# Optimization experiments

Hardware: AMD Instinct MI355X
Metric: run time of the kernel (lower is better)

Reference implementation:

```python
import jax, jax.numpy as jnp
import numpy as np

B, N, DM, H, FF = 8, 2048, 1024, 16, 4096
D = DM // H // 2  # head_dim = 32
LAMBDA_INIT = 0.8 - 0.6 * float(np.exp(-0.3 * 1.0))  # layer_num=1


def _layernorm(x, g, b, eps=1e-5):
    mu = jnp.mean(x, axis=-1, keepdims=True)
    var = jnp.mean(jnp.square(x - mu), axis=-1, keepdims=True)
    return (x - mu) * jax.lax.rsqrt(var + eps) * g + b


def _rmsnorm(x, eps=1e-5):
    return x * jax.lax.rsqrt(jnp.mean(x * x, axis=-1, keepdims=True) + eps)


def _diff_attn(x, Wq, Wk, Wv, lq1, lq2, lk1, lk2, Wo, bo):
    b, n, d = x.shape
    scale = D ** -0.5
    # rearrange 'b n (h d q) -> b n (q h) d'
    q = (x @ Wq.T).reshape(b, n, H, D, 2).transpose(0, 1, 4, 2, 3).reshape(b, n, 2 * H, D) * scale
    k = (x @ Wk.T).reshape(b, n, H, D, 2).transpose(0, 1, 4, 2, 3).reshape(b, n, 2 * H, D)
    # rearrange 'b n (h d) -> b h n d' with d = 2*head_dim
    v = (x @ Wv.T).reshape(b, n, H, 2 * D).transpose(0, 2, 1, 3)
    # per-position head-vs-head scores: [b, n, 2H, 2H]
    att = jnp.einsum('bnqd,bnkd->bnqk', q, k)
    att = jnp.nan_to_num(att)
    att = jax.nn.softmax(att.astype(jnp.float32), axis=-1)
    lam = jnp.exp(jnp.sum(lq1 * lk1)) - jnp.exp(jnp.sum(lq2 * lk2)) + LAMBDA_INIT
    # rearrange 'b n (q h) (k a) -> q k b n h a'; take [0,0] - lam*[1,1]
    att6 = att.reshape(b, n, 2, H, 2, H)
    att2 = att6[:, :, 0, :, 0, :] - lam * att6[:, :, 1, :, 1, :]  # [b,n,h,a]
    out = jnp.einsum('bnah,bhnd->bnad', att2, v)  # [b,n,H,2D]
    out = _rmsnorm(out) * (1.0 - LAMBDA_INIT)
    out = out.reshape(b, n, d)
    return out @ Wo.T + bo


def setup_inputs() -> dict:
    key = jax.random.key(0)
    ks = jax.random.split(key, 12)
    p = lambda k, sh, s=0.02: jax.random.normal(k, sh, jnp.float32) * s
    return {
        'x': jax.random.normal(ks[0], (B, N, DM), jnp.float32),
        'Wq': p(ks[1], (DM, DM)), 'Wk': p(ks[2], (DM, DM)), 'Wv': p(ks[3], (DM, DM)),
        'lq1': p(ks[4], (D,), 0.1), 'lq2': p(ks[5], (D,), 0.1),
        'lk1': p(ks[6], (D,), 0.1), 'lk2': p(ks[7], (D,), 0.1),
        'Wo': p(ks[8], (DM, DM)), 'bo': jnp.zeros((DM,), jnp.float32),
        'ln1_g': jnp.ones((DM,), jnp.float32), 'ln1_b': jnp.zeros((DM,), jnp.float32),
        'ln2_g': jnp.ones((DM,), jnp.float32), 'ln2_b': jnp.zeros((DM,), jnp.float32),
        'W1': p(ks[9], (FF, DM)), 'b1': jnp.zeros((FF,), jnp.float32),
        'W2': p(ks[10], (DM, FF)), 'b2': jnp.zeros((DM,), jnp.float32),
    }


def reference(x, Wq, Wk, Wv, lq1, lq2, lk1, lk2, Wo, bo, ln1_g, ln1_b, ln2_g, ln2_b, W1, b1, W2, b2):
    # norm_first=True, use_gate=False, dropout=0 (eval), wo_ffn=False
    skip = x
    h = _layernorm(x, ln1_g, ln1_b)
    src2 = _diff_attn(h, Wq, Wk, Wv, lq1, lq2, lk1, lk2, Wo, bo)
    conn = skip + src2
    skip2 = conn
    h2 = _layernorm(conn, ln2_g, ln2_b)
    src3 = jax.nn.relu(h2 @ W1.T + b1) @ W2.T + b2
    return skip2 + src3
```

## Files before the change

kernel.cpp:

```cpp
#include <hip/hip_runtime.h>
#include <cstdint>

#define DM    1024
#define NHEAD 16
#define FFDIM 4096
#define MROWS 16384
#define QKVS  3072

static constexpr float LAMBDA_INIT_F = 0.3555090675909693f;
static constexpr float ONE_MINUS_LI  = 1.0f - 0.3555090675909693f;
static constexpr float QSCALE        = 0.17677669529663687f;

typedef __attribute__((ext_vector_type(8))) short bf16x8;
typedef __attribute__((ext_vector_type(4))) float f32x4;

__device__ __forceinline__ unsigned short f2bf(float f) {
    union { float f; unsigned int i; } w; w.f = f;
    unsigned int x = w.i;
    return (unsigned short)((x + 0x7fffu + ((x >> 16) & 1u)) >> 16);
}
__device__ __forceinline__ float bf2f(unsigned short u) {
    union { unsigned int i; float f; } w; w.i = ((unsigned int)u) << 16; return w.f;
}

__device__ __forceinline__ void load_lds16(const void* gptr, void* lptr) {
    __builtin_amdgcn_global_load_lds(
        (const __attribute__((address_space(1))) unsigned int*)gptr,
        (__attribute__((address_space(3))) unsigned int*)lptr, 16, 0, 0);
}

__global__ __launch_bounds__(256) void cvt6_kernel(const float* __restrict__ Wq,
                                                   const float* __restrict__ Wk,
                                                   const float* __restrict__ Wv,
                                                   const float* __restrict__ Wo,
                                                   const float* __restrict__ W1,
                                                   const float* __restrict__ W2,
                                                   unsigned short* __restrict__ wqkv,
                                                   unsigned short* __restrict__ wo,
                                                   unsigned short* __restrict__ w1,
                                                   unsigned short* __restrict__ w2)
{
    const int b = blockIdx.x;
    const float* src;
    unsigned short* dst;
    int off;
    if (b < 3072)      { src = (b < 1024) ? Wq : (b < 2048) ? Wk : Wv;
                         dst = wqkv + (b >> 10) * (DM * DM);
                         off = (b & 1023) * 1024; }
    else if (b < 4096) { src = Wo; dst = wo; off = (b - 3072) * 1024; }
    else if (b < 8192) { src = W1; dst = w1; off = (b - 4096) * 1024; }
    else               { src = W2; dst = w2; off = (b - 8192) * 1024; }
    const int i = off + threadIdx.x * 4;
    const float4 v = *(const float4*)&src[i];
    ushort4 o;
    o.x = f2bf(v.x); o.y = f2bf(v.y); o.z = f2bf(v.z); o.w = f2bf(v.w);
    *(ushort4*)&dst[i] = o;
}

__global__ __launch_bounds__(256) void ln_kernel(const float* __restrict__ xin,
                                                 const float* __restrict__ g,
                                                 const float* __restrict__ b,
                                                 unsigned short* __restrict__ out)
{
    const int row = blockIdx.x;
    const int tid = threadIdx.x;
    const float* xr = xin + (size_t)row * DM;
    float v[4];
    #pragma unroll
    for (int i = 0; i < 4; ++i) v[i] = xr[tid + 256 * i];
    float s1 = v[0] + v[1] + v[2] + v[3];
    float s2 = v[0]*v[0] + v[1]*v[1] + v[2]*v[2] + v[3]*v[3];
    #pragma unroll
    for (int off = 32; off > 0; off >>= 1) {
        s1 += __shfl_down(s1, off);
        s2 += __shfl_down(s2, off);
    }
    __shared__ float red[8];
    const int wv = tid >> 6;
    if ((tid & 63) == 0) { red[wv] = s1; red[4 + wv] = s2; }
    __syncthreads();
    s1 = red[0] + red[1] + red[2] + red[3];
    s2 = red[4] + red[5] + red[6] + red[7];
    const float mean = s1 * (1.0f / DM);
    const float var  = s2 * (1.0f / DM) - mean * mean;
    const float inv  = rsqrtf(var + 1e-5f);
    #pragma unroll
    for (int i = 0; i < 4; ++i) {
        const int c = tid + 256 * i;
        out[(size_t)row * DM + c] = f2bf((v[i] - mean) * inv * g[c] + b[c]);
    }
}

template<int EPI>
__global__ __launch_bounds__(512, 2) void gemm256(const unsigned short* __restrict__ A,
                                                  const unsigned short* __restrict__ W,
                                                  void* __restrict__ Cout,
                                                  const float* __restrict__ bias,
                                                  const float* __restrict__ resid,
                                                  int M, int N, int K, int ldb)
{
    __shared__ __align__(16) unsigned short Al[2][256][64];
    __shared__ __align__(16) unsigned short Bl[2][256][64];

    const int tid  = threadIdx.x;
    const int lane = tid & 63;
    const int wv   = tid >> 6;
    const int l15  = lane & 15;
    const int q4   = lane >> 4;
    const int wg   = wv >> 2;
    const int cg   = wv & 3;
    const int m0   = blockIdx.y * 256;
    const int n0   = blockIdx.x * 256;
    const int KT   = K >> 6;

    const int sr = tid >> 3;
    const int sc = (tid & 7) ^ (sr & 7);
    const unsigned short* gA = A + (size_t)(m0 + sr) * K   + sc * 8;
    const unsigned short* gB = W + (size_t)(n0 + sr) * ldb + sc * 8;
    const size_t aH = (size_t)128 * K;
    const size_t bH = (size_t)128 * ldb;
    const size_t aC = (size_t)64 * K;
    const size_t bC = (size_t)64 * ldb;
    unsigned short* lA = &Al[0][0][0] + wv * 512;
    unsigned short* lB = &Bl[0][0][0] + wv * 512;

#define STG_A(boff, hoff, gp) do { \
    load_lds16((gp),      lA + (boff) + (hoff)); \
    load_lds16((gp) + aC, lA + (boff) + (hoff) + 4096); } while (0)
#define STG_B(boff, hoff, gp) do { \
    load_lds16((gp),      lB + (boff) + (hoff)); \
    load_lds16((gp) + bC, lB + (boff) + (hoff) + 4096); } while (0)

    STG_A(0, 0,    gA);
    STG_B(0, 0,    gB);
    STG_A(0, 8192, gA + aH);
    STG_B(0, 8192, gB + bH);
    if (KT > 1) {
        STG_A(16384, 0,    gA + 64);
        STG_B(16384, 0,    gB + 64);
        STG_A(16384, 8192, gA + aH + 64);
        asm volatile("s_waitcnt vmcnt(6)" ::: "memory");
    } else {
        asm volatile("s_waitcnt vmcnt(0)" ::: "memory");
    }
    __builtin_amdgcn_s_barrier();
    __builtin_amdgcn_sched_barrier(0);

    const int so0 = ( q4      ^ (l15 & 7)) * 8;
    const int so1 = ((q4 + 4) ^ (l15 & 7)) * 8;
    const unsigned short* rA = &Al[0][wg * 64 + l15][0];
    const unsigned short* rB = &Bl[0][cg * 32 + l15][0];

    const f32x4 fz = {0.f, 0.f, 0.f, 0.f};
    f32x4 acc[8][4];
    #pragma unroll
    for (int i = 0; i < 8; ++i)
        #pragma unroll
        for (int j = 0; j < 4; ++j) acc[i][j] = fz;

    bf16x8 a[4][2], b0[2][2], b1[2][2];

    for (int t = 0; t < KT; ++t) {
        const int bo = (t & 1) << 14;
        const int bn = bo ^ 16384;
        const int k1 = (t + 1) << 6;
        const int k2 = (t + 2) << 6;

        #pragma unroll
        for (int mf = 0; mf < 4; ++mf) {
            a[mf][0] = *(const bf16x8*)&rA[bo + mf * 1024 + so0];
            a[mf][1] = *(const bf16x8*)&rA[bo + mf * 1024 + so1];
        }
        #pragma unroll
        for (int nf = 0; nf < 2; ++nf) {
            b0[nf][0] = *(const bf16x8*)&rB[bo + nf * 1024 + so0];
            b0[nf][1] = *(const bf16x8*)&rB[bo + nf * 1024 + so1];
        }
        if (t + 1 < KT) STG_B(bn, 8192, gB + bH + k1);
        __builtin_amdgcn_s_barrier();
        __builtin_amdgcn_sched_barrier(0);
        __builtin_amdgcn_s_setprio(1);
        #pragma unroll
        for (int mf = 0; mf < 4; ++mf)
            #pragma unroll
            for (int nf = 0; nf < 2; ++nf) {
                acc[mf][nf] = __builtin_amdgcn_mfma_f32_16x16x32_bf16(a[mf][0], b0[nf][0], acc[mf][nf], 0, 0, 0);
                acc[mf][nf] = __builtin_amdgcn_mfma_f32_16x16x32_bf16(a[mf][1], b0[nf][1], acc[mf][nf], 0, 0, 0);
            }
        __builtin_amdgcn_s_setprio(0);
        __builtin_amdgcn_s_barrier();
        __builtin_amdgcn_sched_barrier(0);

        #pragma unroll
        for (int nf = 0; nf < 2; ++nf) {
            b1[nf][0] = *(const bf16x8*)&rB[bo + 8192 + nf * 1024 + so0];
            b1[nf][1] = *(const bf16x8*)&rB[bo + 8192 + nf * 1024 + so1];
        }
        if (t + 2 < KT) STG_A(bo, 0, gA + k2);
        __builtin_amdgcn_s_barrier();
        __builtin_amdgcn_sched_barrier(0);
        __builtin_amdgcn_s_setprio(1);
        #pragma unroll
        for (int mf = 0; mf < 4; ++mf)
            #pragma unroll
            for (int nf = 0; nf < 2; ++nf) {
                acc[mf][2 + nf] = __builtin_amdgcn_mfma_f32_16x16x32_bf16(a[mf][0], b1[nf][0], acc[mf][2 + nf], 0, 0, 0);
                acc[mf][2 + nf] = __builtin_amdgcn_mfma_f32_16x16x32_bf16(a[mf][1], b1[nf][1], acc[mf][2 + nf], 0, 0, 0);
            }
        __builtin_amdgcn_s_setprio(0);
        __builtin_amdgcn_s_barrier();
        __builtin_amdgcn_sched_barrier(0);

        #pragma unroll
        for (int mf = 0; mf < 4; ++mf) {
            a[mf][0] = *(const bf16x8*)&rA[bo + 8192 + mf * 1024 + so0];
            a[mf][1] = *(const bf16x8*)&rA[bo + 8192 + mf * 1024 + so1];
        }
        if (t + 2 < KT) STG_B(bo, 0, gB + k2);
        __builtin_amdgcn_s_barrier();
        __builtin_amdgcn_sched_barrier(0);
        __builtin_amdgcn_s_setprio(1);
        #pragma unroll
        for (int mf = 0; mf < 4; ++mf)
            #pragma unroll
            for (int nf = 0; nf < 2; ++nf) {
                acc[4 + mf][nf] = __builtin_amdgcn_mfma_f32_16x16x32_bf16(a[mf][0], b0[nf][0], acc[4 + mf][nf], 0, 0, 0);
                acc[4 + mf][nf] = __builtin_amdgcn_mfma_f32_16x16x32_bf16(a[mf][1], b0[nf][1], acc[4 + mf][nf], 0, 0, 0);
            }
        __builtin_amdgcn_s_setprio(0);
        __builtin_amdgcn_s_barrier();
        __builtin_amdgcn_sched_barrier(0);

        if (t + 2 < KT) STG_A(bo, 8192, gA + aH + k2);
        __builtin_amdgcn_s_barrier();
        __builtin_amdgcn_sched_barrier(0);
        __builtin_amdgcn_s_setprio(1);
        #pragma unroll
        for (int mf = 0; mf < 4; ++mf)
            #pragma unroll
            for (int nf = 0; nf < 2; ++nf) {
                acc[4 + mf][2 + nf] = __builtin_amdgcn_mfma_f32_16x16x32_bf16(a[mf][0], b1[nf][0], acc[4 + mf][2 + nf], 0, 0, 0);
                acc[4 + mf][2 + nf] = __builtin_amdgcn_mfma_f32_16x16x32_bf16(a[mf][1], b1[nf][1], acc[4 + mf][2 + nf], 0, 0, 0);
            }
        __builtin_amdgcn_s_setprio(0);
        if (t + 2 < KT) {
            asm volatile("s_waitcnt vmcnt(6)" ::: "memory");
        } else if (t + 2 == KT) {
            asm volatile("s_waitcnt vmcnt(0)" ::: "memory");
        }
        if (t + 1 < KT) {
            __builtin_amdgcn_s_barrier();
            __builtin_amdgcn_sched_barrier(0);
        }
    }
#undef STG_A
#undef STG_B

    #pragma unroll
    for (int hm = 0; hm < 2; ++hm)
    #pragma unroll
    for (int mf = 0; mf < 4; ++mf)
    #pragma unroll
    for (int hb = 0; hb < 2; ++hb)
    #pragma unroll
    for (int nf = 0; nf < 2; ++nf)
    #pragma unroll
    for (int rr = 0; rr < 4; ++rr) {
        const int m = m0 + hm * 128 + wg * 64 + mf * 16 + q4 * 4 + rr;
        const int n = n0 + hb * 128 + cg * 32 + nf * 16 + l15;
        const size_t off = (size_t)m * N + n;
        float c = acc[hm * 4 + mf][hb * 2 + nf][rr];
        if (EPI == 0) {
            ((unsigned short*)Cout)[off] = f2bf(c);
        } else if (EPI == 1) {
            ((float*)Cout)[off] = c + bias[n] + resid[off];
        } else if (EPI == 2) {
            ((unsigned short*)Cout)[off] = f2bf(fmaxf(c + bias[n], 0.f));
        } else {
            ((float*)Cout)[off] = c + resid[off];
        }
    }
}

__global__ __launch_bounds__(256) void attn_pos(const unsigned short* __restrict__ qkv,
                                                const float* __restrict__ lq1,
                                                const float* __restrict__ lq2,
                                                const float* __restrict__ lk1,
                                                const float* __restrict__ lk2,
                                                unsigned short* __restrict__ outg)
{
    __shared__ __align__(16) float q2[4][32][36];
    __shared__ __align__(16) float k2[4][32][36];
    __shared__ __align__(16) float v2[4][16][64];
    __shared__ float att2[4][16][17];

    const int tid  = threadIdx.x;
    const int wave = tid >> 6;
    const int lane = tid & 63;
    const int pos  = blockIdx.x * 4 + wave;

    float s1 = 0.f, s2 = 0.f;
    #pragma unroll
    for (int i = 0; i < 32; ++i) {
        s1 += lq1[i] * lk1[i];
        s2 += lq2[i] * lk2[i];
    }
    const float lam = __expf(s1) - __expf(s2) + LAMBDA_INIT_F;

    const unsigned short* qrow = qkv + (size_t)pos * QKVS;
    const unsigned short* krow = qrow + DM;
    const unsigned short* vrow = qrow + 2 * DM;

    unsigned short tq[16], tk[16], tv[16];
    *(uint4*)&tq[0] = *(const uint4*)&qrow[lane * 16];
    *(uint4*)&tq[8] = *(const uint4*)&qrow[lane * 16 + 8];
    *(uint4*)&tk[0] = *(const uint4*)&krow[lane * 16];
    *(uint4*)&tk[8] = *(const uint4*)&krow[lane * 16 + 8];
    *(uint4*)&tv[0] = *(const uint4*)&vrow[lane * 16];
    *(uint4*)&tv[8] = *(const uint4*)&vrow[lane * 16 + 8];

    #pragma unroll
    for (int jj = 0; jj < 16; ++jj) {
        const int c  = lane * 16 + jj;
        const int h  = c >> 6;
        const int d  = (c >> 1) & 31;
        const int qi = c & 1;
        q2[wave][qi * 16 + h][d] = bf2f(tq[jj]) * QSCALE;
        k2[wave][qi * 16 + h][d] = bf2f(tk[jj]);
        v2[wave][c >> 6][c & 63] = bf2f(tv[jj]);
    }
    __syncthreads();

    const int qh = lane & 31, half = lane >> 5;
    float qreg[32];
    #pragma unroll
    for (int d4 = 0; d4 < 32; d4 += 4) {
        const f32x4 t = *(const f32x4*)&q2[wave][qh][d4];
        qreg[d4] = t[0]; qreg[d4+1] = t[1]; qreg[d4+2] = t[2]; qreg[d4+3] = t[3];
    }
    float p[16];
    #pragma unroll
    for (int jj = 0; jj < 16; ++jj) {
        const float* kr = &k2[wave][half * 16 + jj][0];
        float a = 0.f;
        #pragma unroll
        for (int d4 = 0; d4 < 32; d4 += 4) {
            const f32x4 kv = *(const f32x4*)&kr[d4];
            a += qreg[d4]*kv[0] + qreg[d4+1]*kv[1] + qreg[d4+2]*kv[2] + qreg[d4+3]*kv[3];
        }
        p[jj] = a;
    }

    float mx = p[0];
    #pragma unroll
    for (int jj = 1; jj < 16; ++jj) mx = fmaxf(mx, p[jj]);
    mx = fmaxf(mx, __shfl_xor(mx, 32));
    float sum = 0.f;
    #pragma unroll
    for (int jj = 0; jj < 16; ++jj) { p[jj] = __expf(p[jj] - mx); sum += p[jj]; }
    sum += __shfl_xor(sum, 32);
    const float inv = 1.0f / sum;

    if (half == 0 && qh < 16) {
        #pragma unroll
        for (int jj = 0; jj < 16; ++jj) att2[wave][qh][jj] = p[jj] * inv;
    }
    __syncthreads();
    if (half == 1 && qh >= 16) {
        const int a = qh - 16;
        #pragma unroll
        for (int jj = 0; jj < 16; ++jj) att2[wave][a][jj] -= lam * p[jj] * inv;
    }
    __syncthreads();

    const int a   = lane & 15;
    const int ddb = (lane >> 4) * 16;
    float areg[16];
    #pragma unroll
    for (int h = 0; h < 16; ++h) areg[h] = att2[wave][a][h];
    float o[16];
    #pragma unroll
    for (int j = 0; j < 16; ++j) o[j] = 0.f;
    #pragma unroll
    for (int h = 0; h < 16; ++h) {
        #pragma unroll
        for (int j4 = 0; j4 < 16; j4 += 4) {
            const f32x4 vv = *(const f32x4*)&v2[wave][h][ddb + j4];
            o[j4]   += areg[h] * vv[0];
            o[j4+1] += areg[h] * vv[1];
            o[j4+2] += areg[h] * vv[2];
            o[j4+3] += areg[h] * vv[3];
        }
    }

    float ss = 0.f;
    #pragma unroll
    for (int j = 0; j < 16; ++j) ss += o[j] * o[j];
    ss += __shfl_xor(ss, 16);
    ss += __shfl_xor(ss, 32);
    const float scl = rsqrtf(ss * (1.0f / 64.0f) + 1e-5f) * ONE_MINUS_LI;

    unsigned short ob[16];
    #pragma unroll
    for (int j = 0; j < 16; ++j) ob[j] = f2bf(o[j] * scl);
    unsigned short* orow = outg + (size_t)pos * DM + a * 64 + ddb;
    *(uint4*)&orow[0] = *(const uint4*)&ob[0];
    *(uint4*)&orow[8] = *(const uint4*)&ob[8];
}

extern "C" void kernel_launch(void* const* d_in, const int* in_sizes, int n_in,
                              void* d_out, int out_size, void* d_ws, size_t ws_size,
                              hipStream_t stream)
{
    const float* x   = (const float*)d_in[0];
    const float* Wq  = (const float*)d_in[1];
    const float* Wk  = (const float*)d_in[2];
    const float* Wv  = (const float*)d_in[3];
    const float* lq1 = (const float*)d_in[4];
    const float* lq2 = (const float*)d_in[5];
    const float* lk1 = (const float*)d_in[6];
    const float* lk2 = (const float*)d_in[7];
    const float* Wo  = (const float*)d_in[8];
    const float* bo  = (const float*)d_in[9];
    const float* g1  = (const float*)d_in[10];
    const float* be1 = (const float*)d_in[11];
    const float* g2  = (const float*)d_in[12];
    const float* be2 = (const float*)d_in[13];
    const float* W1  = (const float*)d_in[14];
    const float* b1  = (const float*)d_in[15];
    const float* W2  = (const float*)d_in[16];
    const float* b2  = (const float*)d_in[17];
    (void)in_sizes; (void)n_in; (void)out_size;

    const size_t MB = 1ull << 20;
    char* ws = (char*)d_ws;
    unsigned short* wqkv = (unsigned short*)(ws);
    unsigned short* wo   = (unsigned short*)(ws + 6 * MB);
    unsigned short* w1   = (unsigned short*)(ws + 8 * MB);
    unsigned short* w2   = (unsigned short*)(ws + 16 * MB);
    unsigned short* h    = (unsigned short*)(ws + 24 * MB);
    unsigned short* qkv  = (unsigned short*)(ws + 56 * MB);
    float*          conn = (float*)(ws + 56 * MB);
    unsigned short* attn = h;
    unsigned short* h2   = (unsigned short*)(ws + 120 * MB);
    unsigned short* t    = (unsigned short*)(ws + 152 * MB);

    int nf = 1;
    while (nf < 16 && 152 * MB + (size_t)MROWS * (FFDIM / nf) * 2 > ws_size) nf <<= 1;
    const int FC = FFDIM / nf;

    const dim3 b256(256), b512(512);

    cvt6_kernel<<<12288, b256, 0, stream>>>(Wq, Wk, Wv, Wo, W1, W2, wqkv, wo, w1, w2);

    ln_kernel<<<MROWS, b256, 0, stream>>>(x, g1, be1, h);

    gemm256<0><<<dim3(QKVS / 256, MROWS / 256), b512, 0, stream>>>(
        h, wqkv, qkv, nullptr, nullptr, MROWS, QKVS, DM, DM);

    attn_pos<<<MROWS / 4, b256, 0, stream>>>(qkv, lq1, lq2, lk1, lk2, attn);

    gemm256<1><<<dim3(DM / 256, MROWS / 256), b512, 0, stream>>>(
        attn, wo, conn, bo, x, MROWS, DM, DM, DM);

    ln_kernel<<<MROWS, b256, 0, stream>>>(conn, g2, be2, h2);

    for (int c = 0; c < nf; ++c) {
        gemm256<2><<<dim3(FC / 256, MROWS / 256), b512, 0, stream>>>(
            h2, w1 + (size_t)c * FC * DM, t, b1 + c * FC, nullptr, MROWS, FC, DM, DM);
        if (c == 0)
            gemm256<1><<<dim3(DM / 256, MROWS / 256), b512, 0, stream>>>(
                t, w2 + (size_t)c * FC, (float*)d_out, b2, conn, MROWS, DM, FC, FFDIM);
        else
            gemm256<4><<<dim3(DM / 256, MROWS / 256), b512, 0, stream>>>(
                t, w2 + (size_t)c * FC, (float*)d_out, nullptr, (const float*)d_out, MROWS, DM, FC, FFDIM);
    }
}
```

Baseline: 707.8 us.

## Swizzle GEMM block order and drop barriers between LDS reads and MFMA phases

Remaps the linear workgroup index into eight interleaved groups so that concurrently running blocks share A/B tiles and get better L2 reuse. It removes the s_barrier and sched_barrier that sat between each LDS fragment load / global-to-LDS stage and the MFMA cluster that follows, halving the barrier count per k-step. It also reorders the LDS fragment loads so the first MFMA's operands arrive first. Without those barriers the compiler can move loads and MFMAs across phases, and correctness now depends on the remaining barriers still ordering LDS writes against reads.

Result: no change. 698.4 us (-1.3%).

```diff
diff --git a/kernel.cpp b/kernel.cpp
--- a/kernel.cpp
+++ b/kernel.cpp
@@ -109,9 +109,21 @@
     const int q4   = lane >> 4;
     const int wg   = wv >> 2;
     const int cg   = wv & 3;
-    const int m0   = blockIdx.y * 256;
-    const int n0   = blockIdx.x * 256;
-    const int KT   = K >> 6;
+
+    int bx = blockIdx.x, by = blockIdx.y;
+    {
+        const int gx  = gridDim.x;
+        const int nwg = gx * gridDim.y;
+        if ((nwg & 7) == 0) {
+            const int lin = by * gx + bx;
+            const int swz = (lin & 7) * (nwg >> 3) + (lin >> 3);
+            bx = swz % gx;
+            by = swz / gx;
+        }
+    }
+    const int m0 = by * 256;
+    const int n0 = bx * 256;
+    const int KT = K >> 6;
 
     const int sr = tid >> 3;
     const int sc = (tid & 7) ^ (sr & 7);
@@ -166,19 +178,19 @@
         const int k1 = (t + 1) << 6;
         const int k2 = (t + 2) << 6;
 
-        #pragma unroll
-        for (int mf = 0; mf < 4; ++mf) {
-            a[mf][0] = *(const bf16x8*)&rA[bo + mf * 1024 + so0];
-            a[mf][1] = *(const bf16x8*)&rA[bo + mf * 1024 + so1];
-        }
-        #pragma unroll
-        for (int nf = 0; nf < 2; ++nf) {
-            b0[nf][0] = *(const bf16x8*)&rB[bo + nf * 1024 + so0];
-            b0[nf][1] = *(const bf16x8*)&rB[bo + nf * 1024 + so1];
-        }
+        a[0][0]  = *(const bf16x8*)&rA[bo + 0 * 1024 + so0];
+        b0[0][0] = *(const bf16x8*)&rB[bo + 0 * 1024 + so0];
+        a[0][1]  = *(const bf16x8*)&rA[bo + 0 * 1024 + so1];
+        b0[0][1] = *(const bf16x8*)&rB[bo + 0 * 1024 + so1];
+        b0[1][0] = *(const bf16x8*)&rB[bo + 1 * 1024 + so0];
+        b0[1][1] = *(const bf16x8*)&rB[bo + 1 * 1024 + so1];
+        a[1][0]  = *(const bf16x8*)&rA[bo + 1 * 1024 + so0];
+        a[1][1]  = *(const bf16x8*)&rA[bo + 1 * 1024 + so1];
+        a[2][0]  = *(const bf16x8*)&rA[bo + 2 * 1024 + so0];
+        a[2][1]  = *(const bf16x8*)&rA[bo + 2 * 1024 + so1];
+        a[3][0]  = *(const bf16x8*)&rA[bo + 3 * 1024 + so0];
+        a[3][1]  = *(const bf16x8*)&rA[bo + 3 * 1024 + so1];
         if (t + 1 < KT) STG_B(bn, 8192, gB + bH + k1);
-        __builtin_amdgcn_s_barrier();
-        __builtin_amdgcn_sched_barrier(0);
         __builtin_amdgcn_s_setprio(1);
         #pragma unroll
         for (int mf = 0; mf < 4; ++mf)
@@ -191,14 +203,11 @@
         __builtin_amdgcn_s_barrier();
         __builtin_amdgcn_sched_barrier(0);
 
-        #pragma unroll
-        for (int nf = 0; nf < 2; ++nf) {
-            b1[nf][0] = *(const bf16x8*)&rB[bo + 8192 + nf * 1024 + so0];
-            b1[nf][1] = *(const bf16x8*)&rB[bo + 8192 + nf * 1024 + so1];
-        }
+        b1[0][0] = *(const bf16x8*)&rB[bo + 8192 + 0 * 1024 + so0];
+        b1[0][1] = *(const bf16x8*)&rB[bo + 8192 + 0 * 1024 + so1];
+        b1[1][0] = *(const bf16x8*)&rB[bo + 8192 + 1 * 1024 + so0];
+        b1[1][1] = *(const bf16x8*)&rB[bo + 8192 + 1 * 1024 + so1];
         if (t + 2 < KT) STG_A(bo, 0, gA + k2);
-        __builtin_amdgcn_s_barrier();
-        __builtin_amdgcn_sched_barrier(0);
         __builtin_amdgcn_s_setprio(1);
         #pragma unroll
         for (int mf = 0; mf < 4; ++mf)
@@ -211,14 +220,15 @@
         __builtin_amdgcn_s_barrier();
         __builtin_amdgcn_sched_barrier(0);
 
-        #pragma unroll
-        for (int mf = 0; mf < 4; ++mf) {
-            a[mf][0] = *(const bf16x8*)&rA[bo + 8192 + mf * 1024 + so0];
-            a[mf][1] = *(const bf16x8*)&rA[bo + 8192 + mf * 1024 + so1];
-        }
+        a[0][0] = *(const bf16x8*)&rA[bo + 8192 + 0 * 1024 + so0];
+        a[0][1] = *(const bf16x8*)&rA[bo + 8192 + 0 * 1024 + so1];
+        a[1][0] = *(const bf16x8*)&rA[bo + 8192 + 1 * 1024 + so0];
+        a[1][1] = *(const bf16x8*)&rA[bo + 8192 + 1 * 1024 + so1];
+        a[2][0] = *(const bf16x8*)&rA[bo + 8192 + 2 * 1024 + so0];
+        a[2][1] = *(const bf16x8*)&rA[bo + 8192 + 2 * 1024 + so1];
+        a[3][0] = *(const bf16x8*)&rA[bo + 8192 + 3 * 1024 + so0];
+        a[3][1] = *(const bf16x8*)&rA[bo + 8192 + 3 * 1024 + so1];
         if (t + 2 < KT) STG_B(bo, 0, gB + k2);
-        __builtin_amdgcn_s_barrier();
-        __builtin_amdgcn_sched_barrier(0);
         __builtin_amdgcn_s_setprio(1);
         #pragma unroll
         for (int mf = 0; mf < 4; ++mf)
@@ -232,8 +242,6 @@
         __builtin_amdgcn_sched_barrier(0);
 
         if (t + 2 < KT) STG_A(bo, 8192, gA + aH + k2);
-        __builtin_amdgcn_s_barrier();
-        __builtin_amdgcn_sched_barrier(0);
         __builtin_amdgcn_s_setprio(1);
         #pragma unroll
         for (int mf = 0; mf < 4; ++mf)
```

## Restructure GEMM K-loop to prefetch LDS fragments and halve barriers; add XCD tile swizzle

Applied to the files above, without the earlier changes.

Reorders the 256x256 GEMM main loop so each phase issues the LDS fragment reads for the next quadrant while the current MFMA block runs. This cuts the per-iteration barriers from eight to four and loads the first fragments before the loop begins. The B upper-half stage for the next tile moves into the prologue, and global stages are rescheduled to match. It also remaps block indices so consecutive workgroups spread across the 8 XCDs in contiguous chunks, aiming for better L2 reuse. The risks are higher register pressure and more complex hazards on LDS buffer reuse.

Result: slower. 729.8 us (+3.1%).

```diff
diff --git a/kernel.cpp b/kernel.cpp
--- a/kernel.cpp
+++ b/kernel.cpp
@@ -109,9 +109,21 @@
     const int q4   = lane >> 4;
     const int wg   = wv >> 2;
     const int cg   = wv & 3;
-    const int m0   = blockIdx.y * 256;
-    const int n0   = blockIdx.x * 256;
-    const int KT   = K >> 6;
+
+    int bx = blockIdx.x, by = blockIdx.y;
+    {
+        const int gx  = gridDim.x;
+        const int nwg = gx * gridDim.y;
+        if ((nwg & 7) == 0) {
+            const int lin = by * gx + bx;
+            const int swz = (lin & 7) * (nwg >> 3) + (lin >> 3);
+            bx = swz % gx;
+            by = swz / gx;
+        }
+    }
+    const int m0 = by * 256;
+    const int n0 = bx * 256;
+    const int KT = K >> 6;
 
     const int sr = tid >> 3;
     const int sc = (tid & 7) ^ (sr & 7);
@@ -139,7 +151,8 @@
         STG_A(16384, 0,    gA + 64);
         STG_B(16384, 0,    gB + 64);
         STG_A(16384, 8192, gA + aH + 64);
-        asm volatile("s_waitcnt vmcnt(6)" ::: "memory");
+        STG_B(16384, 8192, gB + bH + 64);
+        asm volatile("s_waitcnt vmcnt(8)" ::: "memory");
     } else {
         asm volatile("s_waitcnt vmcnt(0)" ::: "memory");
     }
@@ -158,97 +171,112 @@
         #pragma unroll
         for (int j = 0; j < 4; ++j) acc[i][j] = fz;
 
-    bf16x8 a[4][2], b0[2][2], b1[2][2];
+    bf16x8 af[4][2], b0f[2][2], b1f[2][2];
+
+    #pragma unroll
+    for (int mf = 0; mf < 4; ++mf) {
+        af[mf][0] = *(const bf16x8*)&rA[mf * 1024 + so0];
+        af[mf][1] = *(const bf16x8*)&rA[mf * 1024 + so1];
+    }
+    #pragma unroll
+    for (int nf = 0; nf < 2; ++nf) {
+        b0f[nf][0] = *(const bf16x8*)&rB[nf * 1024 + so0];
+        b0f[nf][1] = *(const bf16x8*)&rB[nf * 1024 + so1];
+    }
+    asm volatile("s_waitcnt lgkmcnt(0)" ::: "memory");
+    __builtin_amdgcn_sched_barrier(0);
+    __builtin_amdgcn_s_barrier();
+    __builtin_amdgcn_sched_barrier(0);
 
     for (int t = 0; t < KT; ++t) {
         const int bo = (t & 1) << 14;
         const int bn = bo ^ 16384;
-        const int k1 = (t + 1) << 6;
         const int k2 = (t + 2) << 6;
 
-        #pragma unroll
-        for (int mf = 0; mf < 4; ++mf) {
-            a[mf][0] = *(const bf16x8*)&rA[bo + mf * 1024 + so0];
-            a[mf][1] = *(const bf16x8*)&rA[bo + mf * 1024 + so1];
-        }
-        #pragma unroll
-        for (int nf = 0; nf < 2; ++nf) {
-            b0[nf][0] = *(const bf16x8*)&rB[bo + nf * 1024 + so0];
-            b0[nf][1] = *(const bf16x8*)&rB[bo + nf * 1024 + so1];
-        }
-        if (t + 1 < KT) STG_B(bn, 8192, gB + bH + k1);
-        __builtin_amdgcn_s_barrier();
+        b1f[0][0] = *(const bf16x8*)&rB[bo + 8192 + 0 * 1024 + so0];
+        b1f[0][1] = *(const bf16x8*)&rB[bo + 8192 + 0 * 1024 + so1];
+        b1f[1][0] = *(const bf16x8*)&rB[bo + 8192 + 1 * 1024 + so0];
+        b1f[1][1] = *(const bf16x8*)&rB[bo + 8192 + 1 * 1024 + so1];
+        if (t + 2 < KT) STG_A(bo, 0, gA + k2);
         __builtin_amdgcn_sched_barrier(0);
         __builtin_amdgcn_s_setprio(1);
         #pragma unroll
         for (int mf = 0; mf < 4; ++mf)
             #pragma unroll
             for (int nf = 0; nf < 2; ++nf) {
-                acc[mf][nf] = __builtin_amdgcn_mfma_f32_16x16x32_bf16(a[mf][0], b0[nf][0], acc[mf][nf], 0, 0, 0);
-                acc[mf][nf] = __builtin_amdgcn_mfma_f32_16x16x32_bf16(a[mf][1], b0[nf][1], acc[mf][nf], 0, 0, 0);
+                acc[mf][nf] = __builtin_amdgcn_mfma_f32_16x16x32_bf16(af[mf][0], b0f[nf][0], acc[mf][nf], 0, 0, 0);
+                acc[mf][nf] = __builtin_amdgcn_mfma_f32_16x16x32_bf16(af[mf][1], b0f[nf][1], acc[mf][nf], 0, 0, 0);
             }
         __builtin_amdgcn_s_setprio(0);
+        asm volatile("s_waitcnt lgkmcnt(0)" ::: "memory");
+        __builtin_amdgcn_sched_barrier(0);
         __builtin_amdgcn_s_barrier();
         __builtin_amdgcn_sched_barrier(0);
 
-        #pragma unroll
-        for (int nf = 0; nf < 2; ++nf) {
-            b1[nf][0] = *(const bf16x8*)&rB[bo + 8192 + nf * 1024 + so0];
-            b1[nf][1] = *(const bf16x8*)&rB[bo + 8192 + nf * 1024 + so1];
-        }
-        if (t + 2 < KT) STG_A(bo, 0, gA + k2);
-        __builtin_amdgcn_s_barrier();
-        __builtin_amdgcn_sched_barrier(0);
+        if (t + 2 < KT) STG_B(bo, 0, gB + k2);
         __builtin_amdgcn_s_setprio(1);
         #pragma unroll
         for (int mf = 0; mf < 4; ++mf)
             #pragma unroll
             for (int nf = 0; nf < 2; ++nf) {
-                acc[mf][2 + nf] = __builtin_amdgcn_mfma_f32_16x16x32_bf16(a[mf][0], b1[nf][0], acc[mf][2 + nf], 0, 0, 0);
-                acc[mf][2 + nf] = __builtin_amdgcn_mfma_f32_16x16x32_bf16(a[mf][1], b1[nf][1], acc[mf][2 + nf], 0, 0, 0);
+                acc[mf][2 + nf] = __builtin_amdgcn_mfma_f32_16x16x32_bf16(af[mf][0], b1f[nf][0], acc[mf][2 + nf], 0, 0, 0);
+                acc[mf][2 + nf] = __builtin_amdgcn_mfma_f32_16x16x32_bf16(af[mf][1], b1f[nf][1], acc[mf][2 + nf], 0, 0, 0);
             }
         __builtin_amdgcn_s_setprio(0);
+        __builtin_amdgcn_sched_barrier(0);
+        #pragma unroll
+        for (int mf = 0; mf < 4; ++mf) {
+            af[mf][0] = *(const bf16x8*)&rA[bo + 8192 + mf * 1024 + so0];
+            af[mf][1] = *(const bf16x8*)&rA[bo + 8192 + mf * 1024 + so1];
+        }
+        asm volatile("s_waitcnt lgkmcnt(0)" ::: "memory");
+        __builtin_amdgcn_sched_barrier(0);
         __builtin_amdgcn_s_barrier();
         __builtin_amdgcn_sched_barrier(0);
 
-        #pragma unroll
-        for (int mf = 0; mf < 4; ++mf) {
-            a[mf][0] = *(const bf16x8*)&rA[bo + 8192 + mf * 1024 + so0];
-            a[mf][1] = *(const bf16x8*)&rA[bo + 8192 + mf * 1024 + so1];
-        }
-        if (t + 2 < KT) STG_B(bo, 0, gB + k2);
-        __builtin_amdgcn_s_barrier();
-        __builtin_amdgcn_sched_barrier(0);
+        if (t + 2 < KT) STG_A(bo, 8192, gA + aH + k2);
         __builtin_amdgcn_s_setprio(1);
         #pragma unroll
         for (int mf = 0; mf < 4; ++mf)
             #pragma unroll
             for (int nf = 0; nf < 2; ++nf) {
-                acc[4 + mf][nf] = __builtin_amdgcn_mfma_f32_16x16x32_bf16(a[mf][0], b0[nf][0], acc[4 + mf][nf], 0, 0, 0);
-                acc[4 + mf][nf] = __builtin_amdgcn_mfma_f32_16x16x32_bf16(a[mf][1], b0[nf][1], acc[4 + mf][nf], 0, 0, 0);
-            }
-        __builtin_amdgcn_s_setprio(0);
-        __builtin_amdgcn_s_barrier();
-        __builtin_amdgcn_sched_barrier(0);
-
-        if (t + 2 < KT) STG_A(bo, 8192, gA + aH + k2);
-        __builtin_amdgcn_s_barrier();
-        __builtin_amdgcn_sched_barrier(0);
-        __builtin_amdgcn_s_setprio(1);
-        #pragma unroll
-        for (int mf = 0; mf < 4; ++mf)
-            #pragma unroll
-            for (int nf = 0; nf < 2; ++nf) {
-                acc[4 + mf][2 + nf] = __builtin_amdgcn_mfma_f32_16x16x32_bf16(a[mf][0], b1[nf][0], acc[4 + mf][2 + nf], 0, 0, 0);
-                acc[4 + mf][2 + nf] = __builtin_amdgcn_mfma_f32_16x16x32_bf16(a[mf][1], b1[nf][1], acc[4 + mf][2 + nf], 0, 0, 0);
+                acc[4 + mf][2 + nf] = __builtin_amdgcn_mfma_f32_16x16x32_bf16(af[mf][0], b1f[nf][0], acc[4 + mf][2 + nf], 0, 0, 0);
+                acc[4 + mf][2 + nf] = __builtin_amdgcn_mfma_f32_16x16x32_bf16(af[mf][1], b1f[nf][1], acc[4 + mf][2 + nf], 0, 0, 0);
             }
         __builtin_amdgcn_s_setprio(0);
         if (t + 2 < KT) {
             asm volatile("s_waitcnt vmcnt(6)" ::: "memory");
-        } else if (t + 2 == KT) {
+        } else {
             asm volatile("s_waitcnt vmcnt(0)" ::: "memory");
         }
+        __builtin_amdgcn_sched_barrier(0);
+        __builtin_amdgcn_s_barrier();
+        __builtin_amdgcn_sched_barrier(0);
+
+        if (t + 2 < KT) STG_B(bo, 8192, gB + bH + k2);
+        __builtin_amdgcn_s_setprio(1);
+        #pragma unroll
+        for (int mf = 0; mf < 4; ++mf)
+            #pragma unroll
+            for (int nf = 0; nf < 2; ++nf) {
+                acc[4 + mf][nf] = __builtin_amdgcn_mfma_f32_16x16x32_bf16(af[mf][0], b0f[nf][0], acc[4 + mf][nf], 0, 0, 0);
+                acc[4 + mf][nf] = __builtin_amdgcn_mfma_f32_16x16x32_bf16(af[mf][1], b0f[nf][1], acc[4 + mf][nf], 0, 0, 0);
+            }
+        __builtin_amdgcn_s_setprio(0);
+        __builtin_amdgcn_sched_barrier(0);
         if (t + 1 < KT) {
+            #pragma unroll
+            for (int mf = 0; mf < 4; ++mf) {
+                af[mf][0] = *(const bf16x8*)&rA[bn + mf * 1024 + so0];
+                af[mf][1] = *(const bf16x8*)&rA[bn + mf * 1024 + so1];
+            }
+            #pragma unroll
+            for (int nf = 0; nf < 2; ++nf) {
+                b0f[nf][0] = *(const bf16x8*)&rB[bn + nf * 1024 + so0];
+                b0f[nf][1] = *(const bf16x8*)&rB[bn + nf * 1024 + so1];
+            }
+            asm volatile("s_waitcnt lgkmcnt(0)" ::: "memory");
+            __builtin_amdgcn_sched_barrier(0);
             __builtin_amdgcn_s_barrier();
             __builtin_amdgcn_sched_barrier(0);
         }
```
